# Kernel tuning notes

Hardware: AMD Instinct MI355X
Metric: run time of the kernel (lower is better)

Reference implementation:

```python
import jax, jax.numpy as jnp
import numpy as np

D = 768
HEAD_SIZE = 64  # D // 12


def setup_inputs() -> dict:
    key = jax.random.key(0)
    k_ix, k_wk, k_wq, k_wv = jax.random.split(key, 4)
    ix = jax.random.normal(k_ix, (4, 4096, D), dtype=jnp.float32)
    s = 1.0 / np.sqrt(D)
    Wk = jax.random.normal(k_wk, (D, HEAD_SIZE), dtype=jnp.float32) * s
    Wq = jax.random.normal(k_wq, (D, HEAD_SIZE), dtype=jnp.float32) * s
    Wv = jax.random.normal(k_wv, (D, HEAD_SIZE), dtype=jnp.float32) * s
    return {"ix": ix, "Wk": Wk, "Wq": Wq, "Wv": Wv}


def reference(ix, Wk, Wq, Wv):
    # ix: [B, N, D]; W*: [D, h]
    k = ix @ Wk            # [B, N, h]
    q = ix @ Wq            # [B, N, h]
    v = ix @ Wv            # [B, N, h]
    scale = HEAD_SIZE ** -0.5
    wei = jnp.einsum('bnh,bmh->bnm', q, k) * scale  # [B, N, N]
    wei = jax.nn.softmax(wei, axis=-1)
    out = jnp.einsum('bnm,bmh->bnh', wei, v)        # [B, N, h]
    return out
```

## Files before the change

### kernel.cpp

```cpp
#include <hip/hip_runtime.h>
#include <math.h>

#define Dm   768
#define Hm   64
#define SEQ  4096
#define NB   4
#define NROW (NB * SEQ)

#define QSCALE (0.125f * 1.4426950408889634f)

typedef _Float16 f16;
typedef __attribute__((ext_vector_type(8))) _Float16 f16x8;
typedef __attribute__((ext_vector_type(2))) __fp16 fp16x2_raw;
typedef __attribute__((ext_vector_type(4))) float f32x4;
typedef unsigned int uint;
typedef unsigned short ushort;

#define MFMAH(A, B, C) __builtin_amdgcn_mfma_f32_16x16x32_f16(A, B, C, 0, 0, 0)

__device__ __forceinline__ uint pkrtz(float a, float b) {
    fp16x2_raw r = __builtin_amdgcn_cvt_pkrtz(a, b);
    return __builtin_bit_cast(uint, r);
}
__device__ __forceinline__ ushort f2h(float f) {
    f16 h = (f16)f;
    return __builtin_bit_cast(ushort, h);
}
union F16x8U { uint u[4]; f16x8 v; };

__global__ __launch_bounds__(256) void wconv(
    const float* __restrict__ Wq, const float* __restrict__ Wk,
    const float* __restrict__ Wv, ushort* __restrict__ WTt)
{
    const int c   = blockIdx.x;
    const int mat = c >> 6, col = c & 63;
    const float* W = (mat == 0) ? Wq : (mat == 1 ? Wk : Wv);
    const float sc = (mat == 0) ? QSCALE : 1.0f;
    for (int k = threadIdx.x; k < Dm; k += 256)
        WTt[((size_t)(k >> 5) * 192 + c) * 32 + (k & 31)] = f2h(W[k * 64 + col] * sc);
}

__global__ __launch_bounds__(256) void proj(
    const float* __restrict__ ix, const ushort* __restrict__ WTt,
    ushort* __restrict__ Qw, ushort* __restrict__ Kt, ushort* __restrict__ Vt)
{
    __shared__ __align__(16) float comb[2][3072];

    const int t    = threadIdx.x;
    const int lane = t & 63;
    const int w    = __builtin_amdgcn_readfirstlane(t >> 6);
    const int rt   = w & 1, kh = w >> 1;
    const int q15  = lane & 15, quad = lane >> 4;
    const int gr0  = blockIdx.x * 32;
    const int row  = gr0 + rt * 16 + q15;

    const float*  Ab = ix + (size_t)row * Dm + kh * 384 + quad * 8;
    const ushort* Bb = WTt + ((size_t)(kh * 12) * 192 + q15) * 32 + quad * 8;

    f32x4 acc[12];
#pragma unroll
    for (int ct = 0; ct < 12; ++ct) acc[ct] = (f32x4){0.f, 0.f, 0.f, 0.f};

    f32x4 Af[2][2];
    Af[0][0] = *(const f32x4*)(Ab);
    Af[0][1] = *(const f32x4*)(Ab + 4);

#pragma unroll 2
    for (int it = 0; it < 12; ++it) {
        const int cur = it & 1, nxt = cur ^ 1;

        f16x8 Bf[12];
#pragma unroll
        for (int ct = 0; ct < 12; ++ct)
            Bf[ct] = *(const f16x8*)(Bb + (size_t)it * 6144 + ct * 512);

        if (it < 11) {
            Af[nxt][0] = *(const f32x4*)(Ab + (it + 1) * 32);
            Af[nxt][1] = *(const f32x4*)(Ab + (it + 1) * 32 + 4);
        }

        F16x8U af;
        af.u[0] = pkrtz(Af[cur][0].x, Af[cur][0].y);
        af.u[1] = pkrtz(Af[cur][0].z, Af[cur][0].w);
        af.u[2] = pkrtz(Af[cur][1].x, Af[cur][1].y);
        af.u[3] = pkrtz(Af[cur][1].z, Af[cur][1].w);
#pragma unroll
        for (int ct = 0; ct < 12; ++ct)
            acc[ct] = MFMAH(af.v, Bf[ct], acc[ct]);
    }

    if (kh == 1) {
#pragma unroll
        for (int ct = 0; ct < 12; ++ct)
            *(f32x4*)&comb[rt][(ct * 64 + lane) * 4] = acc[ct];
    }
    __syncthreads();
    if (kh == 0) {
#pragma unroll
        for (int ct = 0; ct < 12; ++ct) {
            f32x4 o = *(const f32x4*)&comb[rt][(ct * 64 + lane) * 4];
            acc[ct].x += o.x; acc[ct].y += o.y; acc[ct].z += o.z; acc[ct].w += o.w;
        }
        const int n4  = (gr0 >> 4) + rt;
        const int j32 = gr0 >> 5;
#pragma unroll
        for (int ct = 0; ct < 12; ++ct) {
            float vals[4] = {acc[ct].x, acc[ct].y, acc[ct].z, acc[ct].w};
            if (ct < 4) {
#pragma unroll
                for (int r = 0; r < 4; ++r)
                    Qw[(size_t)(gr0 + rt * 16 + quad * 4 + r) * 64 + ct * 16 + q15] = f2h(vals[r]);
            } else if (ct < 8) {
#pragma unroll
                for (int r = 0; r < 4; ++r)
                    Kt[(size_t)n4 * 1024 + (ct - 4) * 256 + (quad * 4 + r) * 16 + q15] = f2h(vals[r]);
            } else {
                ushort4 vv;
                vv.x = f2h(vals[0]); vv.y = f2h(vals[1]);
                vv.z = f2h(vals[2]); vv.w = f2h(vals[3]);
                *(ushort4*)(Vt + (size_t)j32 * 2048 + (ct - 8) * 512 +
                            (rt * 2 + (quad >> 1)) * 128 + q15 * 8 + (quad & 1) * 4) = vv;
            }
        }
    }
}

__global__ __launch_bounds__(512, 2) void attn(
    const ushort* __restrict__ Qw, const ushort* __restrict__ Kt,
    const ushort* __restrict__ Vt, float* __restrict__ out)
{
    __shared__ __align__(16) float aF[16896];
    short* aS = (short*)aF;

    const int t    = threadIdx.x;
    const int lane = t & 63;
    const int w    = __builtin_amdgcn_readfirstlane(t >> 6);
    const int q15  = lane & 15, quad = lane >> 4;

    const int bb    = blockIdx.x;
    const int xcd   = bb & 7;
    const int batch = xcd >> 1;
    const int slot  = (bb >> 3) | ((xcd & 1) << 5);
    const int q0    = slot * 64;
    const size_t base = (size_t)batch * SEQ;

    f16x8 qf[4][2];
#pragma unroll
    for (int g = 0; g < 4; ++g)
#pragma unroll
        for (int h = 0; h < 2; ++h)
            qf[g][h] = *(const f16x8*)(Qw + (base + q0 + g * 16 + q15) * 64 + h * 32 + quad * 8);

    f32x4 oacc[4][4];
#pragma unroll
    for (int g = 0; g < 4; ++g)
#pragma unroll
        for (int dt = 0; dt < 4; ++dt) oacc[g][dt] = (f32x4){0.f, 0.f, 0.f, 0.f};
    float lsum[4] = {0.f, 0.f, 0.f, 0.f};

    const size_t j0g = base + w * 512;
    const ushort* Kfb = Kt + (j0g >> 4) * 1024;
    const ushort* Vfb = Vt + (j0g >> 5) * 2048 + lane * 8;
    short* Ps = aS + w * 2560;

    int koff[2][2];
#pragma unroll
    for (int jt = 0; jt < 2; ++jt)
#pragma unroll
        for (int h = 0; h < 2; ++h)
            koff[jt][h] = jt * 1024 + h * 512 + (quad >> 1) * 256 + q15 * 16 + (quad & 1) * 8;

    f16x8 kf[2][2][2], vf[2][4];
#pragma unroll
    for (int jt = 0; jt < 2; ++jt)
#pragma unroll
        for (int h = 0; h < 2; ++h)
            kf[0][jt][h] = *(const f16x8*)(Kfb + koff[jt][h]);
#pragma unroll
    for (int dt = 0; dt < 4; ++dt)
        vf[0][dt] = *(const f16x8*)(Vfb + dt * 512);

#pragma unroll 2
    for (int it = 0; it < 16; ++it) {
        const int cur = it & 1, nxt = cur ^ 1;
        if (it < 15) {
#pragma unroll
            for (int jt = 0; jt < 2; ++jt)
#pragma unroll
                for (int h = 0; h < 2; ++h)
                    kf[nxt][jt][h] = *(const f16x8*)(Kfb + (size_t)(it + 1) * 2048 + koff[jt][h]);
#pragma unroll
            for (int dt = 0; dt < 4; ++dt)
                vf[nxt][dt] = *(const f16x8*)(Vfb + (size_t)(it + 1) * 2048 + dt * 512);
        }

#pragma unroll
        for (int g = 0; g < 4; ++g) {
#pragma unroll
            for (int jt = 0; jt < 2; ++jt) {
                f32x4 z = (f32x4){0.f, 0.f, 0.f, 0.f};
                z = MFMAH(kf[cur][jt][0], qf[g][0], z);
                z = MFMAH(kf[cur][jt][1], qf[g][1], z);
                float e0 = exp2f(z.x), e1 = exp2f(z.y);
                float e2 = exp2f(z.z), e3 = exp2f(z.w);
                lsum[g] += (e0 + e1) + (e2 + e3);
                uint2 pk = make_uint2(pkrtz(e0, e1), pkrtz(e2, e3));
                *(uint2*)(Ps + (g * 16 + q15) * 40 + jt * 16 + quad * 4) = pk;
            }
        }

        f16x8 pf[4];
#pragma unroll
        for (int g = 0; g < 4; ++g)
            pf[g] = *(const f16x8*)(Ps + (g * 16 + q15) * 40 + quad * 8);
#pragma unroll
        for (int dt = 0; dt < 4; ++dt)
#pragma unroll
            for (int g = 0; g < 4; ++g)
                oacc[g][dt] = MFMAH(pf[g], vf[cur][dt], oacc[g][dt]);
    }

#pragma unroll
    for (int g = 0; g < 4; ++g) {
        lsum[g] += __shfl_xor(lsum[g], 16);
        lsum[g] += __shfl_xor(lsum[g], 32);
    }
    if (quad == 0) {
#pragma unroll
        for (int g = 0; g < 4; ++g)
            aF[16384 + w * 64 + g * 16 + q15] = lsum[g];
    }
    __syncthreads();

#define OWRITE(idx)                                                          \
    {                                                                        \
        float* b = aF + (idx) * 4096;                                        \
        _Pragma("unroll") for (int g = 0; g < 4; ++g)                        \
        _Pragma("unroll") for (int dt = 0; dt < 4; ++dt) {                   \
            b[(g * 16 + quad * 4 + 0) * 64 + dt * 16 + q15] = oacc[g][dt].x; \
            b[(g * 16 + quad * 4 + 1) * 64 + dt * 16 + q15] = oacc[g][dt].y; \
            b[(g * 16 + quad * 4 + 2) * 64 + dt * 16 + q15] = oacc[g][dt].z; \
            b[(g * 16 + quad * 4 + 3) * 64 + dt * 16 + q15] = oacc[g][dt].w; \
        }                                                                    \
    }
#define OADD(idx)                                                            \
    {                                                                        \
        const float* b = aF + (idx) * 4096;                                  \
        _Pragma("unroll") for (int g = 0; g < 4; ++g)                        \
        _Pragma("unroll") for (int dt = 0; dt < 4; ++dt) {                   \
            oacc[g][dt].x += b[(g * 16 + quad * 4 + 0) * 64 + dt * 16 + q15];\
            oacc[g][dt].y += b[(g * 16 + quad * 4 + 1) * 64 + dt * 16 + q15];\
            oacc[g][dt].z += b[(g * 16 + quad * 4 + 2) * 64 + dt * 16 + q15];\
            oacc[g][dt].w += b[(g * 16 + quad * 4 + 3) * 64 + dt * 16 + q15];\
        }                                                                    \
    }
    if (w >= 4) OWRITE(w - 4);
    __syncthreads();
    if (w < 4) OADD(w);
    __syncthreads();
    if (w == 2 || w == 3) OWRITE(w - 2);
    __syncthreads();
    if (w < 2) OADD(w);
    __syncthreads();
    if (w < 2) OWRITE(w);
    __syncthreads();

    {
        const int q  = t >> 3;
        const int d0 = (t & 7) * 8;
        float l = 0.f;
#pragma unroll
        for (int i = 0; i < 8; ++i) l += aF[16384 + i * 64 + q];
        const float linv = 1.0f / l;
#pragma unroll
        for (int k2 = 0; k2 < 2; ++k2) {
            float4 a = *(const float4*)&aF[q * 64 + d0 + k2 * 4];
            float4 b = *(const float4*)&aF[4096 + q * 64 + d0 + k2 * 4];
            float4 s;
            s.x = (a.x + b.x) * linv; s.y = (a.y + b.y) * linv;
            s.z = (a.z + b.z) * linv; s.w = (a.w + b.w) * linv;
            *(float4*)(out + (base + q0 + q) * 64 + d0 + k2 * 4) = s;
        }
    }
}

extern "C" void kernel_launch(void* const* d_in, const int* in_sizes, int n_in,
                              void* d_out, int out_size, void* d_ws, size_t ws_size,
                              hipStream_t stream)
{
    const float* ix = (const float*)d_in[0];
    const float* Wk = (const float*)d_in[1];
    const float* Wq = (const float*)d_in[2];
    const float* Wv = (const float*)d_in[3];
    float* out = (float*)d_out;

    ushort* Qw  = (ushort*)d_ws;
    ushort* Kt  = Qw + (size_t)NROW * Hm;
    ushort* Vt  = Kt + (size_t)NROW * Hm;
    ushort* WTt = Vt + (size_t)NROW * Hm;

    wconv<<<192, 256, 0, stream>>>(Wq, Wk, Wv, WTt);
    proj<<<512, 256, 0, stream>>>(ix, WTt, Qw, Kt, Vt);
    attn<<<256, 512, 0, stream>>>(Qw, Kt, Vt, out);
}
```

Baseline: 135.9 us.

## Software-pipeline attention QK/PV stages and split projection K-dimension four ways

The attention loop becomes a three-stage software pipeline. K/V loads run two iterations ahead, and QK^T plus exp for the next tile is issued before the PV MFMAs of the current tile. This uses double-buffered P tiles in shared memory, which enlarges LDS to 84KB per block. The projection kernel now gives each block 16 rows, splits the 768-wide reduction across 4 waves with a two-stage LDS reduction, doubles the grid, and uses a 3-deep A prefetch. The aim is to hide latency and raise occupancy, at the cost of more registers, more LDS and extra syncs.

```diff
diff --git a/kernel.cpp b/kernel.cpp
--- a/kernel.cpp
+++ b/kernel.cpp
@@ -40,7 +40,7 @@
         WTt[((size_t)(k >> 5) * 192 + c) * 32 + (k & 31)] = f2h(W[k * 64 + col] * sc);
 }
 
-__global__ __launch_bounds__(256) void proj(
+__global__ __launch_bounds__(256, 3) void proj(
     const float* __restrict__ ix, const ushort* __restrict__ WTt,
     ushort* __restrict__ Qw, ushort* __restrict__ Kt, ushort* __restrict__ Vt)
 {
@@ -48,60 +48,74 @@
 
     const int t    = threadIdx.x;
     const int lane = t & 63;
-    const int w    = __builtin_amdgcn_readfirstlane(t >> 6);
-    const int rt   = w & 1, kh = w >> 1;
+    const int kh   = __builtin_amdgcn_readfirstlane(t >> 6);
     const int q15  = lane & 15, quad = lane >> 4;
-    const int gr0  = blockIdx.x * 32;
-    const int row  = gr0 + rt * 16 + q15;
-
-    const float*  Ab = ix + (size_t)row * Dm + kh * 384 + quad * 8;
-    const ushort* Bb = WTt + ((size_t)(kh * 12) * 192 + q15) * 32 + quad * 8;
+    const int gr0  = blockIdx.x * 16;
+
+    const float*  Ab = ix + (size_t)(gr0 + q15) * Dm + kh * 192 + quad * 8;
+    const ushort* Bb = WTt + ((size_t)(kh * 6) * 192 + q15) * 32 + quad * 8;
 
     f32x4 acc[12];
 #pragma unroll
     for (int ct = 0; ct < 12; ++ct) acc[ct] = (f32x4){0.f, 0.f, 0.f, 0.f};
 
-    f32x4 Af[2][2];
-    Af[0][0] = *(const f32x4*)(Ab);
-    Af[0][1] = *(const f32x4*)(Ab + 4);
-
-#pragma unroll 2
-    for (int it = 0; it < 12; ++it) {
-        const int cur = it & 1, nxt = cur ^ 1;
-
+    f32x4 Af[3][2];
+#pragma unroll
+    for (int i = 0; i < 2; ++i) {
+        Af[i][0] = *(const f32x4*)(Ab + i * 32);
+        Af[i][1] = *(const f32x4*)(Ab + i * 32 + 4);
+    }
+
+#pragma unroll
+    for (int it = 0; it < 6; ++it) {
         f16x8 Bf[12];
 #pragma unroll
         for (int ct = 0; ct < 12; ++ct)
             Bf[ct] = *(const f16x8*)(Bb + (size_t)it * 6144 + ct * 512);
 
-        if (it < 11) {
-            Af[nxt][0] = *(const f32x4*)(Ab + (it + 1) * 32);
-            Af[nxt][1] = *(const f32x4*)(Ab + (it + 1) * 32 + 4);
+        if (it + 2 < 6) {
+            Af[(it + 2) % 3][0] = *(const f32x4*)(Ab + (it + 2) * 32);
+            Af[(it + 2) % 3][1] = *(const f32x4*)(Ab + (it + 2) * 32 + 4);
         }
 
         F16x8U af;
-        af.u[0] = pkrtz(Af[cur][0].x, Af[cur][0].y);
-        af.u[1] = pkrtz(Af[cur][0].z, Af[cur][0].w);
-        af.u[2] = pkrtz(Af[cur][1].x, Af[cur][1].y);
-        af.u[3] = pkrtz(Af[cur][1].z, Af[cur][1].w);
+        af.u[0] = pkrtz(Af[it % 3][0].x, Af[it % 3][0].y);
+        af.u[1] = pkrtz(Af[it % 3][0].z, Af[it % 3][0].w);
+        af.u[2] = pkrtz(Af[it % 3][1].x, Af[it % 3][1].y);
+        af.u[3] = pkrtz(Af[it % 3][1].z, Af[it % 3][1].w);
 #pragma unroll
         for (int ct = 0; ct < 12; ++ct)
             acc[ct] = MFMAH(af.v, Bf[ct], acc[ct]);
     }
 
+    if (kh >= 2) {
+#pragma unroll
+        for (int ct = 0; ct < 12; ++ct)
+            *(f32x4*)&comb[kh - 2][(ct * 64 + lane) * 4] = acc[ct];
+    }
+    __syncthreads();
+    if (kh < 2) {
+#pragma unroll
+        for (int ct = 0; ct < 12; ++ct) {
+            f32x4 o = *(const f32x4*)&comb[kh][(ct * 64 + lane) * 4];
+            acc[ct].x += o.x; acc[ct].y += o.y; acc[ct].z += o.z; acc[ct].w += o.w;
+        }
+    }
+    __syncthreads();
     if (kh == 1) {
 #pragma unroll
         for (int ct = 0; ct < 12; ++ct)
-            *(f32x4*)&comb[rt][(ct * 64 + lane) * 4] = acc[ct];
+            *(f32x4*)&comb[0][(ct * 64 + lane) * 4] = acc[ct];
     }
     __syncthreads();
     if (kh == 0) {
 #pragma unroll
         for (int ct = 0; ct < 12; ++ct) {
-            f32x4 o = *(const f32x4*)&comb[rt][(ct * 64 + lane) * 4];
+            f32x4 o = *(const f32x4*)&comb[0][(ct * 64 + lane) * 4];
             acc[ct].x += o.x; acc[ct].y += o.y; acc[ct].z += o.z; acc[ct].w += o.w;
         }
-        const int n4  = (gr0 >> 4) + rt;
+        const int h16 = (gr0 >> 4) & 1;
+        const int n4  = gr0 >> 4;
         const int j32 = gr0 >> 5;
 #pragma unroll
         for (int ct = 0; ct < 12; ++ct) {
@@ -109,7 +123,7 @@
             if (ct < 4) {
 #pragma unroll
                 for (int r = 0; r < 4; ++r)
-                    Qw[(size_t)(gr0 + rt * 16 + quad * 4 + r) * 64 + ct * 16 + q15] = f2h(vals[r]);
+                    Qw[(size_t)(gr0 + quad * 4 + r) * 64 + ct * 16 + q15] = f2h(vals[r]);
             } else if (ct < 8) {
 #pragma unroll
                 for (int r = 0; r < 4; ++r)
@@ -119,7 +133,7 @@
                 vv.x = f2h(vals[0]); vv.y = f2h(vals[1]);
                 vv.z = f2h(vals[2]); vv.w = f2h(vals[3]);
                 *(ushort4*)(Vt + (size_t)j32 * 2048 + (ct - 8) * 512 +
-                            (rt * 2 + (quad >> 1)) * 128 + q15 * 8 + (quad & 1) * 4) = vv;
+                            (h16 * 2 + (quad >> 1)) * 128 + q15 * 8 + (quad & 1) * 4) = vv;
             }
         }
     }
@@ -129,7 +143,7 @@
     const ushort* __restrict__ Qw, const ushort* __restrict__ Kt,
     const ushort* __restrict__ Vt, float* __restrict__ out)
 {
-    __shared__ __align__(16) float aF[16896];
+    __shared__ __align__(16) float aF[20992];
     short* aS = (short*)aF;
 
     const int t    = threadIdx.x;
@@ -161,7 +175,7 @@
     const size_t j0g = base + w * 512;
     const ushort* Kfb = Kt + (j0g >> 4) * 1024;
     const ushort* Vfb = Vt + (j0g >> 5) * 2048 + lane * 8;
-    short* Ps = aS + w * 2560;
+    short* Ps = aS + w * 5120;
 
     int koff[2][2];
 #pragma unroll
@@ -170,54 +184,48 @@
         for (int h = 0; h < 2; ++h)
             koff[jt][h] = jt * 1024 + h * 512 + (quad >> 1) * 256 + q15 * 16 + (quad & 1) * 8;
 
-    f16x8 kf[2][2][2], vf[2][4];
-#pragma unroll
-    for (int jt = 0; jt < 2; ++jt)
-#pragma unroll
-        for (int h = 0; h < 2; ++h)
-            kf[0][jt][h] = *(const f16x8*)(Kfb + koff[jt][h]);
-#pragma unroll
-    for (int dt = 0; dt < 4; ++dt)
-        vf[0][dt] = *(const f16x8*)(Vfb + dt * 512);
-
-#pragma unroll 2
-    for (int it = 0; it < 16; ++it) {
-        const int cur = it & 1, nxt = cur ^ 1;
-        if (it < 15) {
-#pragma unroll
-            for (int jt = 0; jt < 2; ++jt)
-#pragma unroll
-                for (int h = 0; h < 2; ++h)
-                    kf[nxt][jt][h] = *(const f16x8*)(Kfb + (size_t)(it + 1) * 2048 + koff[jt][h]);
-#pragma unroll
-            for (int dt = 0; dt < 4; ++dt)
-                vf[nxt][dt] = *(const f16x8*)(Vfb + (size_t)(it + 1) * 2048 + dt * 512);
-        }
-
-#pragma unroll
-        for (int g = 0; g < 4; ++g) {
-#pragma unroll
-            for (int jt = 0; jt < 2; ++jt) {
-                f32x4 z = (f32x4){0.f, 0.f, 0.f, 0.f};
-                z = MFMAH(kf[cur][jt][0], qf[g][0], z);
-                z = MFMAH(kf[cur][jt][1], qf[g][1], z);
-                float e0 = exp2f(z.x), e1 = exp2f(z.y);
-                float e2 = exp2f(z.z), e3 = exp2f(z.w);
-                lsum[g] += (e0 + e1) + (e2 + e3);
-                uint2 pk = make_uint2(pkrtz(e0, e1), pkrtz(e2, e3));
-                *(uint2*)(Ps + (g * 16 + q15) * 40 + jt * 16 + quad * 4) = pk;
-            }
-        }
-
-        f16x8 pf[4];
-#pragma unroll
-        for (int g = 0; g < 4; ++g)
-            pf[g] = *(const f16x8*)(Ps + (g * 16 + q15) * 40 + quad * 8);
-#pragma unroll
-        for (int dt = 0; dt < 4; ++dt)
-#pragma unroll
-            for (int g = 0; g < 4; ++g)
-                oacc[g][dt] = MFMAH(pf[g], vf[cur][dt], oacc[g][dt]);
+    f16x8 kf[3][2][2], vf[3][4];
+
+#define LOADKV(slotc, i)                                                       \
+    {                                                                          \
+        _Pragma("unroll") for (int jt = 0; jt < 2; ++jt)                       \
+        _Pragma("unroll") for (int h = 0; h < 2; ++h)                          \
+            kf[slotc][jt][h] = *(const f16x8*)(Kfb + (size_t)(i) * 2048 + koff[jt][h]); \
+        _Pragma("unroll") for (int dt = 0; dt < 4; ++dt)                       \
+            vf[slotc][dt] = *(const f16x8*)(Vfb + (size_t)(i) * 2048 + dt * 512); \
+    }
+#define QKSTEP(slotc, pb)                                                      \
+    {                                                                          \
+        _Pragma("unroll") for (int g = 0; g < 4; ++g)                          \
+        _Pragma("unroll") for (int jt = 0; jt < 2; ++jt) {                     \
+            f32x4 z = (f32x4){0.f, 0.f, 0.f, 0.f};                             \
+            z = MFMAH(kf[slotc][jt][0], qf[g][0], z);                          \
+            z = MFMAH(kf[slotc][jt][1], qf[g][1], z);                          \
+            float e0 = exp2f(z.x), e1 = exp2f(z.y);                            \
+            float e2 = exp2f(z.z), e3 = exp2f(z.w);                            \
+            lsum[g] += (e0 + e1) + (e2 + e3);                                  \
+            uint2 pk = make_uint2(pkrtz(e0, e1), pkrtz(e2, e3));               \
+            *(uint2*)(Ps + (pb) * 2560 + (g * 16 + q15) * 40 + jt * 16 + quad * 4) = pk; \
+        }                                                                      \
+    }
+#define PVSTEP(slotc, pb)                                                      \
+    {                                                                          \
+        f16x8 pf[4];                                                           \
+        _Pragma("unroll") for (int g = 0; g < 4; ++g)                          \
+            pf[g] = *(const f16x8*)(Ps + (pb) * 2560 + (g * 16 + q15) * 40 + quad * 8); \
+        _Pragma("unroll") for (int dt = 0; dt < 4; ++dt)                       \
+        _Pragma("unroll") for (int g = 0; g < 4; ++g)                          \
+            oacc[g][dt] = MFMAH(pf[g], vf[slotc][dt], oacc[g][dt]);            \
+    }
+
+    LOADKV(0, 0);
+    LOADKV(1, 1);
+    QKSTEP(0, 0);
+#pragma unroll
+    for (int i = 0; i < 16; ++i) {
+        if (i + 2 < 16) LOADKV((i + 2) % 3, i + 2);
+        if (i + 1 < 16) QKSTEP((i + 1) % 3, (i + 1) & 1);
+        PVSTEP(i % 3, i & 1);
     }
 
 #pragma unroll
@@ -228,7 +236,7 @@
     if (quad == 0) {
 #pragma unroll
         for (int g = 0; g < 4; ++g)
-            aF[16384 + w * 64 + g * 16 + q15] = lsum[g];
+            aF[20480 + w * 64 + g * 16 + q15] = lsum[g];
     }
     __syncthreads();
 
@@ -270,7 +278,7 @@
         const int d0 = (t & 7) * 8;
         float l = 0.f;
 #pragma unroll
-        for (int i = 0; i < 8; ++i) l += aF[16384 + i * 64 + q];
+        for (int i = 0; i < 8; ++i) l += aF[20480 + i * 64 + q];
         const float linv = 1.0f / l;
 #pragma unroll
         for (int k2 = 0; k2 < 2; ++k2) {
@@ -300,6 +308,6 @@
     ushort* WTt = Vt + (size_t)NROW * Hm;
 
     wconv<<<192, 256, 0, stream>>>(Wq, Wk, Wv, WTt);
-    proj<<<512, 256, 0, stream>>>(ix, WTt, Qw, Kt, Vt);
+    proj<<<1024, 256, 0, stream>>>(ix, WTt, Qw, Kt, Vt);
     attn<<<256, 512, 0, stream>>>(Qw, Kt, Vt, out);
 }
```

Result: no change. 135.5 us (-0.3%).
